# Performance work log

Measured on AMD Instinct MI355X. Metric: run time of the kernel, lower is better.

## Reference

```python
import jax, jax.numpy as jnp
import numpy as np

B, S, DIM = 2, 8192, 1024
NH, NKV, HD = 16, 4, 64
GROUPS = NH // NKV
CHUNK = 128
THETA = 10000.0


def _slopes(h):
    # ALiBi-style per-head decay slopes (h is a power of two)
    return jnp.asarray([2.0 ** (-8.0 / h * (i + 1)) for i in range(h)], dtype=jnp.float32)


def _rope_tables(s, d):
    inv = 1.0 / (THETA ** (np.arange(0, d, 2, dtype=np.float64) / d))
    freqs = np.outer(np.arange(s, dtype=np.float64), inv)  # [s, d/2]
    emb = np.concatenate([freqs, freqs], axis=-1)  # [s, d]
    return jnp.asarray(np.cos(emb), jnp.float32), jnp.asarray(np.sin(emb), jnp.float32)


def _apply_rope(x, cos, sin):
    # x: [b, h, s, d]; cos/sin: [s, d]
    x1, x2 = jnp.split(x, 2, axis=-1)
    rot = jnp.concatenate([-x2, x1], axis=-1)
    return x * cos + rot * sin


def _lightning_attn(q, k, v, slopes, chunk):
    # out[t] = sum_{i<=t} exp(-slope*(t-i)) * (q_t . k_i) * v_i, chunked O(n) recurrence
    b, h, s, d = q.shape
    nc = s // chunk
    t = jnp.arange(chunk, dtype=jnp.float32)
    sl = slopes[:, None, None]  # [h,1,1]
    mask = jnp.where(t[:, None] >= t[None, :],
                     jnp.exp(-sl * (t[:, None] - t[None, :])), 0.0)  # [h,C,C]
    q_dec = jnp.exp(-slopes[:, None] * (t + 1.0))[..., None]          # [h,C,1]
    k_dec = jnp.exp(-slopes[:, None] * (chunk - 1.0 - t))[..., None]  # [h,C,1]
    blk_dec = jnp.exp(-slopes * chunk)[None, :, None, None]           # [1,h,1,1]

    def to_chunks(x):
        return x.reshape(b, h, nc, chunk, d).transpose(2, 0, 1, 3, 4)  # [nc,b,h,C,d]

    qc, kc, vc = to_chunks(q), to_chunks(k), to_chunks(v)

    def step(kv, inp):
        qi, ki, vi = inp  # [b,h,C,d]
        scores = jnp.einsum('bhtd,bhsd->bhts', qi, ki) * mask
        o = jnp.einsum('bhts,bhsd->bhtd', scores, vi) \
            + jnp.einsum('bhtd,bhde->bhte', qi * q_dec, kv)
        kv = blk_dec * kv + jnp.einsum('bhtd,bhte->bhde', ki * k_dec, vi)
        return kv, o

    kv0 = jnp.zeros((b, h, d, d), q.dtype)
    _, outs = jax.lax.scan(step, kv0, (qc, kc, vc))  # outs: [nc,b,h,C,d]
    return outs.transpose(1, 2, 0, 3, 4).reshape(b, h, s, d)


def setup_inputs() -> dict:
    key = jax.random.key(0)
    k0, k1, k2, k3, k4 = jax.random.split(key, 5)
    x = jax.random.normal(k0, (B, S, DIM), jnp.float32)
    Wq = jax.random.normal(k1, (NH * HD, DIM), jnp.float32) * 0.02
    Wk = jax.random.normal(k2, (NKV * HD, DIM), jnp.float32) * 0.02
    Wv = jax.random.normal(k3, (NKV * HD, DIM), jnp.float32) * 0.02
    Wo = jax.random.normal(k4, (DIM, NH * HD), jnp.float32) * 0.02
    return {"x": x, "Wq": Wq, "Wk": Wk, "Wv": Wv, "Wo": Wo}


def reference(x, Wq, Wk, Wv, Wo):
    b, s, _ = x.shape
    q = (x @ Wq.T).reshape(b, s, NH, HD).transpose(0, 2, 1, 3)
    k = (x @ Wk.T).reshape(b, s, NKV, HD).transpose(0, 2, 1, 3)
    v = (x @ Wv.T).reshape(b, s, NKV, HD).transpose(0, 2, 1, 3)
    cos, sin = _rope_tables(s, HD)
    q = _apply_rope(q, cos, sin)
    k = _apply_rope(k, cos, sin)
    # GQA expand: head index = kv_head*groups + g  <=>  repeat along head axis
    k = jnp.repeat(k, GROUPS, axis=1)
    v = jnp.repeat(v, GROUPS, axis=1)
    out = _lightning_attn(q, k, v, _slopes(NH), CHUNK)  # [b,NH,s,HD]
    out = out.transpose(0, 2, 1, 3).reshape(b, s, NH * HD)
    return out @ Wo.T
```

## Files before the change

### kernel.cpp

```cpp
#include <hip/hip_runtime.h>
#include <hip/hip_bf16.h>

#define B_ 2
#define S_ 8192
#define DIM_ 1024
#define NH_ 16
#define NKV_ 4
#define HD_ 64
#define NC_ 64

typedef __bf16 bf16x8 __attribute__((ext_vector_type(8)));
typedef float f32x4 __attribute__((ext_vector_type(4)));
using bf16 = __hip_bfloat16;

#define ASYNC16(gp, lp) __builtin_amdgcn_global_load_lds( \
    (__attribute__((address_space(1))) void*)(void*)(gp), \
    (__attribute__((address_space(3))) void*)(void*)(lp), 16, 0, 0)

__global__ __launch_bounds__(256) void prep_kernel(const float* __restrict__ x, const float* __restrict__ Wq,
                                                   const float* __restrict__ Wk, const float* __restrict__ Wv,
                                                   const float* __restrict__ Wo, bf16* __restrict__ xb,
                                                   bf16* __restrict__ wqkv, bf16* __restrict__ wo,
                                                   float* __restrict__ cosd, float* __restrict__ sind) {
    int bid = blockIdx.x;
    if (bid < 16384) {
        size_t i = ((size_t)bid * 256 + threadIdx.x) * 4;
        const float4 f = *(const float4*)(x + i);
        bf16 t[4];
        t[0] = __float2bfloat16(f.x); t[1] = __float2bfloat16(f.y);
        t[2] = __float2bfloat16(f.z); t[3] = __float2bfloat16(f.w);
        *(uint2*)(xb + i) = *(const uint2*)t;
    } else if (bid < 18944) {
        size_t e = ((size_t)(bid - 16384) * 256 + threadIdx.x) * 4;
        const float* src;
        bf16* dst;
        if (e < 1048576)        { src = Wq + e;             dst = wqkv + e; }
        else if (e < 1310720)   { src = Wk + (e - 1048576); dst = wqkv + e; }
        else if (e < 1572864)   { src = Wv + (e - 1310720); dst = wqkv + e; }
        else                    { src = Wo + (e - 1572864); dst = wo + (e - 1572864); }
        const float4 f = *(const float4*)src;
        bf16 t[4];
        t[0] = __float2bfloat16(f.x); t[1] = __float2bfloat16(f.y);
        t[2] = __float2bfloat16(f.z); t[3] = __float2bfloat16(f.w);
        *(uint2*)dst = *(const uint2*)t;
    } else {
        int idx = (bid - 18944) * 256 + threadIdx.x;
        int s = idx >> 5, i = idx & 31;
        double inv = exp((double)i * (-9.210340371976184 / 32.0));
        double rev = ((double)s * inv) * 0.15915494309189535;
        double frac = rev - floor(rev);
        float a = (float)frac * 6.2831853071795865f;
        cosd[idx] = __cosf(a);
        sind[idx] = __sinf(a);
    }
}

template <typename OT>
__global__ __launch_bounds__(256, 3) void gemm_bt_kernel(const bf16* __restrict__ A, const bf16* __restrict__ Bm,
                                                         OT* __restrict__ C, int M, int N, int K, int rope_ncols,
                                                         const float* __restrict__ cosd,
                                                         const float* __restrict__ sind) {
    __shared__ bf16 As[128 * 64];
    __shared__ bf16 Bs[128 * 64];
    const int tid = threadIdx.x;
    const int bm = blockIdx.x * 128, bn = blockIdx.y * 128;
    const int wave = tid >> 6, lane = tid & 63;
    const int wm = (wave >> 1) * 64, wn = (wave & 1) * 64;
    const int lr = lane & 15, quad = lane >> 4;
    const int srow = wave * 32;
    const int lrow = lane >> 3;
    const int lchunk = ((lane & 7) ^ lrow) * 8;
    const bf16* Ag = A + (size_t)(bm + srow + lrow) * K + lchunk;
    const bf16* Bg = Bm + (size_t)(bn + srow + lrow) * K + lchunk;
    f32x4 acc[4][4] = {};
    for (int k0 = 0; k0 < K; k0 += 64) {
#pragma unroll
        for (int p = 0; p < 4; ++p) {
            ASYNC16(Ag + (size_t)(p * 8) * K + k0, &As[(srow + p * 8) * 64]);
            ASYNC16(Bg + (size_t)(p * 8) * K + k0, &Bs[(srow + p * 8) * 64]);
        }
        __syncthreads();
#pragma unroll
        for (int kk = 0; kk < 64; kk += 32) {
            const int sw = (((kk >> 3) + quad) ^ (lr & 7)) << 3;
            bf16x8 af[4], bfr[4];
#pragma unroll
            for (int i = 0; i < 4; ++i) af[i] = *(const bf16x8*)(&As[(wm + i * 16 + lr) * 64 + sw]);
#pragma unroll
            for (int i = 0; i < 4; ++i) bfr[i] = *(const bf16x8*)(&Bs[(wn + i * 16 + lr) * 64 + sw]);
#pragma unroll
            for (int mi = 0; mi < 4; ++mi)
#pragma unroll
                for (int ni = 0; ni < 4; ++ni)
                    acc[mi][ni] = __builtin_amdgcn_mfma_f32_16x16x32_bf16(af[mi], bfr[ni], acc[mi][ni], 0, 0, 0);
        }
        __syncthreads();
    }
    if (bn + wn < rope_ncols) {
#pragma unroll
        for (int mi = 0; mi < 4; ++mi)
#pragma unroll
            for (int r = 0; r < 4; ++r) {
                int row = bm + wm + mi * 16 + quad * 4 + r;
                int s = row & (S_ - 1);
#pragma unroll
                for (int ni = 0; ni < 2; ++ni) {
                    int i = ni * 16 + lr;
                    float cs = cosd[(s << 5) + i];
                    float sn = sind[(s << 5) + i];
                    float x1 = acc[mi][ni][r], x2 = acc[mi][ni + 2][r];
                    acc[mi][ni][r] = x1 * cs - x2 * sn;
                    acc[mi][ni + 2][r] = x2 * cs + x1 * sn;
                }
            }
    }
#pragma unroll
    for (int mi = 0; mi < 4; ++mi)
#pragma unroll
        for (int ni = 0; ni < 4; ++ni)
#pragma unroll
            for (int r = 0; r < 4; ++r) {
                int row = bm + wm + mi * 16 + quad * 4 + r;
                int col = bn + wn + ni * 16 + lr;
                float v = acc[mi][ni][r];
                if constexpr (__is_same(OT, float)) C[(size_t)row * N + col] = v;
                else C[(size_t)row * N + col] = __float2bfloat16(v);
            }
}


__global__ __launch_bounds__(512) void chunk_kv_kernel(const bf16* __restrict__ qkv, bf16* __restrict__ Cout) {
    const int j = blockIdx.x, g = blockIdx.y, b = blockIdx.z;
    __shared__ bf16 kT[64 * 136];
    __shared__ bf16 vT[64 * 136];
    const int tid = threadIdx.x;
#pragma unroll
    for (int p = 0; p < 2; ++p) {
        int flat = p * 512 + tid;
        int t = flat >> 3, d0 = (flat & 7) * 8;
        const size_t row = (size_t)(b * S_ + j * 128 + t);
        uint4 kw = *(const uint4*)(qkv + row * 1536 + 1024 + g * 64 + d0);
        uint4 vw = *(const uint4*)(qkv + row * 1536 + 1280 + g * 64 + d0);
        const bf16* kp = (const bf16*)&kw;
        const bf16* vp = (const bf16*)&vw;
#pragma unroll
        for (int i = 0; i < 8; ++i) {
            int e = d0 + i;
            int sw = (((t >> 3) & ~7) << 3) + ((((t >> 3) ^ (e >> 3)) & 7) << 3) + (t & 7);
            kT[e * 136 + sw] = kp[i];
            vT[e * 136 + sw] = vp[i];
        }
    }
    __syncthreads();
    const int wave = tid >> 6, lane = tid & 63, lr = lane & 15, quad = lane >> 4;
    const int eblk = (wave & 3) * 16;
    const int hp = (wave >> 2) * 2;
    f32x4 acc[2][4] = {};
    float slope[2], g1[2];
#pragma unroll
    for (int hh = 0; hh < 2; ++hh) {
        slope[hh] = exp2f(-0.5f * (float)(g * 4 + hp + hh + 1));
        g1[hh] = __expf(slope[hh]);
    }
#pragma unroll
    for (int ks = 0; ks < 128; ks += 32) {
        int qa = (ks >> 3) + quad;
        int qhi = (qa & ~7) << 3;
        int ea = eblk + lr;
        bf16x8 a = *(const bf16x8*)(&vT[ea * 136 + qhi + (((qa ^ (ea >> 3)) & 7) << 3)]);
        float av[8];
#pragma unroll
        for (int i = 0; i < 8; ++i) av[i] = (float)a[i];
        bf16x8 bb[4];
#pragma unroll
        for (int ni = 0; ni < 4; ++ni) {
            int eb = ni * 16 + lr;
            bb[ni] = *(const bf16x8*)(&kT[eb * 136 + qhi + (((qa ^ (eb >> 3)) & 7) << 3)]);
        }
#pragma unroll
        for (int hh = 0; hh < 2; ++hh) {
            float m = __expf(-slope[hh] * (float)(127 - ks - quad * 8));
            bf16x8 as;
#pragma unroll
            for (int i = 0; i < 8; ++i) { as[i] = (__bf16)(av[i] * m); m *= g1[hh]; }
#pragma unroll
            for (int ni = 0; ni < 4; ++ni)
                acc[hh][ni] = __builtin_amdgcn_mfma_f32_16x16x32_bf16(as, bb[ni], acc[hh][ni], 0, 0, 0);
        }
    }
#pragma unroll
    for (int hh = 0; hh < 2; ++hh) {
        int h = g * 4 + hp + hh;
        bf16* out = Cout + ((size_t)((b * NH_ + h) * NC_ + j)) * 4096;
#pragma unroll
        for (int ni = 0; ni < 4; ++ni)
#pragma unroll
            for (int r = 0; r < 4; ++r)
                out[(eblk + quad * 4 + r) * 64 + ni * 16 + lr] = __float2bfloat16(acc[hh][ni][r]);
    }
}

__global__ __launch_bounds__(256) void scan_kv_kernel(const bf16* __restrict__ Cin, bf16* __restrict__ st) {
    const int bh = blockIdx.x >> 4;
    const int f = ((blockIdx.x & 15) << 8) + threadIdx.x;
    const int h = bh & (NH_ - 1);
    const float slope = exp2f(-0.5f * (float)(h + 1));
    const float bdec = __expf(-slope * 128.0f);
    const bf16* Cb = Cin + (size_t)bh * NC_ * 4096 + f;
    bf16* sb = st + (size_t)bh * NC_ * 4096 + f;
    float carry = 0.f;
#pragma unroll 8
    for (int c = 0; c < NC_; ++c) {
        sb[(size_t)c * 4096] = __float2bfloat16(carry);
        carry = bdec * carry + __bfloat162float(Cb[(size_t)c * 4096]);
    }
}

__global__ __launch_bounds__(256, 3) void attn_chunk_kernel(const bf16* __restrict__ qkv,
                                                            const bf16* __restrict__ kvst,
                                                            bf16* __restrict__ outb) {
    const int c = blockIdx.x, h = blockIdx.y, b = blockIdx.z;
    const int g = h >> 2;
    const float slope = exp2f(-0.5f * (float)(h + 1));
    __shared__ bf16 smem[26112];
    bf16* qs  = smem;
    bf16* kbs = smem + 8192;
    bf16* Ps  = smem;
    bf16* vT  = smem + 17408;
    const int tid = threadIdx.x;
    const int wave = tid >> 6, lane = tid & 63, lr = lane & 15, quad = lane >> 4;
    const int srow = lane >> 3;
    const int schunk = ((lane & 7) ^ srow) * 8;
#pragma unroll
    for (int p = 0; p < 4; ++p) {
        int t0 = wave * 8 + p * 32;
        size_t row = (size_t)(b * S_ + c * 128 + t0 + srow);
        ASYNC16(qkv + row * 1536 + h * 64 + schunk, &qs[t0 * 64]);
        ASYNC16(qkv + row * 1536 + 1024 + g * 64 + schunk, &kbs[t0 * 64]);
    }
    asm volatile("s_waitcnt vmcnt(0)");
    __syncthreads();
    const int m0 = wave * 32;
    f32x4 sacc[2][8] = {};
#pragma unroll
    for (int kk = 0; kk < 64; kk += 32) {
        const int sw = ((((kk >> 3) + quad) ^ (lr & 7)) & 7) << 3;
        bf16x8 af0 = *(const bf16x8*)(&qs[(m0 + lr) * 64 + sw]);
        bf16x8 af1 = *(const bf16x8*)(&qs[(m0 + 16 + lr) * 64 + sw]);
#pragma unroll
        for (int ni = 0; ni < 8; ++ni) {
            bf16x8 bfr = *(const bf16x8*)(&kbs[(ni * 16 + lr) * 64 + sw]);
            sacc[0][ni] = __builtin_amdgcn_mfma_f32_16x16x32_bf16(af0, bfr, sacc[0][ni], 0, 0, 0);
            sacc[1][ni] = __builtin_amdgcn_mfma_f32_16x16x32_bf16(af1, bfr, sacc[1][ni], 0, 0, 0);
        }
    }
    f32x4 oacc[2][4] = {};
    const bf16* kvb = kvst + ((size_t)((b * NH_ + h) * NC_ + c)) * 4096;
    float qd0 = __expf(-slope * (float)(m0 + lr + 1));
    float qd1 = __expf(-slope * (float)(m0 + 16 + lr + 1));
#pragma unroll
    for (int kk = 0; kk < 64; kk += 32) {
        const int sw = ((((kk >> 3) + quad) ^ (lr & 7)) & 7) << 3;
        bf16x8 a0 = *(const bf16x8*)(&qs[(m0 + lr) * 64 + sw]);
        bf16x8 a1 = *(const bf16x8*)(&qs[(m0 + 16 + lr) * 64 + sw]);
#pragma unroll
        for (int i = 0; i < 8; ++i) {
            a0[i] = (__bf16)((float)a0[i] * qd0);
            a1[i] = (__bf16)((float)a1[i] * qd1);
        }
#pragma unroll
        for (int ni = 0; ni < 4; ++ni) {
            bf16x8 bk = *(const bf16x8*)(kvb + (ni * 16 + lr) * 64 + kk + quad * 8);
            oacc[0][ni] = __builtin_amdgcn_mfma_f32_16x16x32_bf16(a0, bk, oacc[0][ni], 0, 0, 0);
            oacc[1][ni] = __builtin_amdgcn_mfma_f32_16x16x32_bf16(a1, bk, oacc[1][ni], 0, 0, 0);
        }
    }
    __syncthreads();
    float ftv[2][4], gtv[8];
#pragma unroll
    for (int mi = 0; mi < 2; ++mi)
#pragma unroll
        for (int r = 0; r < 4; ++r) ftv[mi][r] = __expf(-slope * (float)(mi * 16 + quad * 4 + r));
#pragma unroll
    for (int ni = 0; ni < 8; ++ni)
        gtv[ni] = __expf(-slope * fmaxf((float)(m0 - (ni * 16 + lr)), -31.0f));
#pragma unroll
    for (int mi = 0; mi < 2; ++mi)
#pragma unroll
        for (int ni = 0; ni < 8; ++ni)
#pragma unroll
            for (int r = 0; r < 4; ++r) {
                int t = m0 + mi * 16 + quad * 4 + r;
                int tp = ni * 16 + lr;
                float val = (t >= tp) ? sacc[mi][ni][r] * ftv[mi][r] * gtv[ni] : 0.f;
                int sw = (((tp >> 3) & ~7) << 3) + ((((tp >> 3) ^ (t >> 3)) & 7) << 3) + (tp & 7);
                Ps[t * 136 + sw] = __float2bfloat16(val);
            }
#pragma unroll
    for (int p = 0; p < 4; ++p) {
        int flat = p * 256 + tid;
        int t = flat >> 3, d0 = (flat & 7) * 8;
        size_t row = (size_t)(b * S_ + c * 128 + t);
        uint4 vw = *(const uint4*)(qkv + row * 1536 + 1280 + g * 64 + d0);
        const bf16* vp = (const bf16*)&vw;
#pragma unroll
        for (int i = 0; i < 8; ++i) {
            int e = d0 + i;
            int sw = (((t >> 3) & ~7) << 3) + ((((t >> 3) ^ (e >> 3)) & 7) << 3) + (t & 7);
            vT[e * 136 + sw] = vp[i];
        }
    }
    __syncthreads();
#pragma unroll
    for (int ks2 = 0; ks2 < 128; ks2 += 32) {
        int qa = (ks2 >> 3) + quad;
        int qhi = (qa & ~7) << 3;
        int ra0 = m0 + lr, ra1 = m0 + 16 + lr;
        bf16x8 af0 = *(const bf16x8*)(&Ps[ra0 * 136 + qhi + (((qa ^ (ra0 >> 3)) & 7) << 3)]);
        bf16x8 af1 = *(const bf16x8*)(&Ps[ra1 * 136 + qhi + (((qa ^ (ra1 >> 3)) & 7) << 3)]);
#pragma unroll
        for (int ni = 0; ni < 4; ++ni) {
            int eb = ni * 16 + lr;
            bf16x8 bfv = *(const bf16x8*)(&vT[eb * 136 + qhi + (((qa ^ (eb >> 3)) & 7) << 3)]);
            oacc[0][ni] = __builtin_amdgcn_mfma_f32_16x16x32_bf16(af0, bfv, oacc[0][ni], 0, 0, 0);
            oacc[1][ni] = __builtin_amdgcn_mfma_f32_16x16x32_bf16(af1, bfv, oacc[1][ni], 0, 0, 0);
        }
    }
#pragma unroll
    for (int mi = 0; mi < 2; ++mi)
#pragma unroll
        for (int ni = 0; ni < 4; ++ni)
#pragma unroll
            for (int r = 0; r < 4; ++r) {
                int t = m0 + mi * 16 + quad * 4 + r;
                int e = ni * 16 + lr;
                size_t row = (size_t)(b * S_ + c * 128 + t);
                outb[row * (NH_ * 64) + h * 64 + e] = __float2bfloat16(oacc[mi][ni][r]);
            }
}

extern "C" void kernel_launch(void* const* d_in, const int* in_sizes, int n_in,
                              void* d_out, int out_size, void* d_ws, size_t ws_size,
                              hipStream_t stream) {
    (void)in_sizes; (void)n_in; (void)out_size; (void)ws_size;
    const float* x  = (const float*)d_in[0];
    const float* Wq = (const float*)d_in[1];
    const float* Wk = (const float*)d_in[2];
    const float* Wv = (const float*)d_in[3];
    const float* Wo = (const float*)d_in[4];
    float* out = (float*)d_out;
    char* ws = (char*)d_ws;
    bf16*  xb    = (bf16*)(ws);
    bf16*  qkvb  = (bf16*)(ws + 33554432);
    bf16*  wqkvb = (bf16*)(ws + 83886080);
    bf16*  wob   = (bf16*)(ws + 87031808);
    float* cosd  = (float*)(ws + 89128960);
    float* sind  = (float*)(ws + 90177536);
    bf16*  Cbuf  = (bf16*)(ws + 91226112);
    bf16*  kvst  = (bf16*)(ws + 108003328);
    bf16*  attn  = xb;

    prep_kernel<<<19968, 256, 0, stream>>>(x, Wq, Wk, Wv, Wo, xb, wqkvb, wob, cosd, sind);

    gemm_bt_kernel<bf16><<<dim3(128, 12), 256, 0, stream>>>(xb, wqkvb, qkvb, 16384, 1536, 1024, 1280, cosd, sind);

    chunk_kv_kernel<<<dim3(NC_, NKV_, B_), 512, 0, stream>>>(qkvb, Cbuf);
    scan_kv_kernel<<<512, 256, 0, stream>>>(Cbuf, kvst);
    attn_chunk_kernel<<<dim3(NC_, NH_, B_), 256, 0, stream>>>(qkvb, kvst, attn);

    gemm_bt_kernel<float><<<dim3(128, 8), 256, 0, stream>>>(attn, wob, out, 16384, 1024, 1024, 0, cosd, sind);
}
```

Before: 264.1 us.

## Split attn chunk kernel across 8 waves with 16-row tiles and early V prefetch

```diff
diff --git a/kernel.cpp b/kernel.cpp
--- a/kernel.cpp
+++ b/kernel.cpp
@@ -216,7 +216,7 @@
     }
 }
 
-__global__ __launch_bounds__(256, 3) void attn_chunk_kernel(const bf16* __restrict__ qkv,
+__global__ __launch_bounds__(512, 2) void attn_chunk_kernel(const bf16* __restrict__ qkv,
                                                             const bf16* __restrict__ kvst,
                                                             bf16* __restrict__ outb) {
     const int c = blockIdx.x, h = blockIdx.y, b = blockIdx.z;
@@ -231,78 +231,74 @@
     const int wave = tid >> 6, lane = tid & 63, lr = lane & 15, quad = lane >> 4;
     const int srow = lane >> 3;
     const int schunk = ((lane & 7) ^ srow) * 8;
-#pragma unroll
-    for (int p = 0; p < 4; ++p) {
-        int t0 = wave * 8 + p * 32;
+    uint4 vreg[2];
+#pragma unroll
+    for (int p = 0; p < 2; ++p) {
+        int flat = p * 512 + tid;
+        int t = flat >> 3, d0 = (flat & 7) * 8;
+        size_t row = (size_t)(b * S_ + c * 128 + t);
+        vreg[p] = *(const uint4*)(qkv + row * 1536 + 1280 + g * 64 + d0);
+    }
+#pragma unroll
+    for (int p = 0; p < 2; ++p) {
+        int t0 = (wave + p * 8) * 8;
         size_t row = (size_t)(b * S_ + c * 128 + t0 + srow);
         ASYNC16(qkv + row * 1536 + h * 64 + schunk, &qs[t0 * 64]);
         ASYNC16(qkv + row * 1536 + 1024 + g * 64 + schunk, &kbs[t0 * 64]);
     }
     asm volatile("s_waitcnt vmcnt(0)");
     __syncthreads();
-    const int m0 = wave * 32;
-    f32x4 sacc[2][8] = {};
-#pragma unroll
-    for (int kk = 0; kk < 64; kk += 32) {
-        const int sw = ((((kk >> 3) + quad) ^ (lr & 7)) & 7) << 3;
-        bf16x8 af0 = *(const bf16x8*)(&qs[(m0 + lr) * 64 + sw]);
-        bf16x8 af1 = *(const bf16x8*)(&qs[(m0 + 16 + lr) * 64 + sw]);
+    const int m0 = wave * 16;
+    bf16x8 qf[2];
+#pragma unroll
+    for (int kk = 0; kk < 2; ++kk)
+        qf[kk] = *(const bf16x8*)(&qs[(m0 + lr) * 64 + ((((kk * 4 + quad)) ^ (lr & 7)) & 7) * 8]);
+    f32x4 sacc[8] = {};
+#pragma unroll
+    for (int kk = 0; kk < 2; ++kk) {
+        const int sw = (((kk * 4 + quad) ^ (lr & 7)) & 7) << 3;
 #pragma unroll
         for (int ni = 0; ni < 8; ++ni) {
             bf16x8 bfr = *(const bf16x8*)(&kbs[(ni * 16 + lr) * 64 + sw]);
-            sacc[0][ni] = __builtin_amdgcn_mfma_f32_16x16x32_bf16(af0, bfr, sacc[0][ni], 0, 0, 0);
-            sacc[1][ni] = __builtin_amdgcn_mfma_f32_16x16x32_bf16(af1, bfr, sacc[1][ni], 0, 0, 0);
-        }
-    }
-    f32x4 oacc[2][4] = {};
+            sacc[ni] = __builtin_amdgcn_mfma_f32_16x16x32_bf16(qf[kk], bfr, sacc[ni], 0, 0, 0);
+        }
+    }
+    f32x4 oacc[4] = {};
     const bf16* kvb = kvst + ((size_t)((b * NH_ + h) * NC_ + c)) * 4096;
-    float qd0 = __expf(-slope * (float)(m0 + lr + 1));
-    float qd1 = __expf(-slope * (float)(m0 + 16 + lr + 1));
-#pragma unroll
-    for (int kk = 0; kk < 64; kk += 32) {
-        const int sw = ((((kk >> 3) + quad) ^ (lr & 7)) & 7) << 3;
-        bf16x8 a0 = *(const bf16x8*)(&qs[(m0 + lr) * 64 + sw]);
-        bf16x8 a1 = *(const bf16x8*)(&qs[(m0 + 16 + lr) * 64 + sw]);
-#pragma unroll
-        for (int i = 0; i < 8; ++i) {
-            a0[i] = (__bf16)((float)a0[i] * qd0);
-            a1[i] = (__bf16)((float)a1[i] * qd1);
-        }
+    float qd = __expf(-slope * (float)(m0 + lr + 1));
+#pragma unroll
+    for (int kk = 0; kk < 2; ++kk) {
+        bf16x8 a0;
+#pragma unroll
+        for (int i = 0; i < 8; ++i) a0[i] = (__bf16)((float)qf[kk][i] * qd);
 #pragma unroll
         for (int ni = 0; ni < 4; ++ni) {
-            bf16x8 bk = *(const bf16x8*)(kvb + (ni * 16 + lr) * 64 + kk + quad * 8);
-            oacc[0][ni] = __builtin_amdgcn_mfma_f32_16x16x32_bf16(a0, bk, oacc[0][ni], 0, 0, 0);
-            oacc[1][ni] = __builtin_amdgcn_mfma_f32_16x16x32_bf16(a1, bk, oacc[1][ni], 0, 0, 0);
+            bf16x8 bk = *(const bf16x8*)(kvb + (ni * 16 + lr) * 64 + kk * 32 + quad * 8);
+            oacc[ni] = __builtin_amdgcn_mfma_f32_16x16x32_bf16(a0, bk, oacc[ni], 0, 0, 0);
         }
     }
     __syncthreads();
-    float ftv[2][4], gtv[8];
-#pragma unroll
-    for (int mi = 0; mi < 2; ++mi)
-#pragma unroll
-        for (int r = 0; r < 4; ++r) ftv[mi][r] = __expf(-slope * (float)(mi * 16 + quad * 4 + r));
+    float ftv[4], gtv[8];
+#pragma unroll
+    for (int r = 0; r < 4; ++r) ftv[r] = __expf(-slope * (float)(quad * 4 + r));
 #pragma unroll
     for (int ni = 0; ni < 8; ++ni)
-        gtv[ni] = __expf(-slope * fmaxf((float)(m0 - (ni * 16 + lr)), -31.0f));
-#pragma unroll
-    for (int mi = 0; mi < 2; ++mi)
-#pragma unroll
-        for (int ni = 0; ni < 8; ++ni)
-#pragma unroll
-            for (int r = 0; r < 4; ++r) {
-                int t = m0 + mi * 16 + quad * 4 + r;
-                int tp = ni * 16 + lr;
-                float val = (t >= tp) ? sacc[mi][ni][r] * ftv[mi][r] * gtv[ni] : 0.f;
-                int sw = (((tp >> 3) & ~7) << 3) + ((((tp >> 3) ^ (t >> 3)) & 7) << 3) + (tp & 7);
-                Ps[t * 136 + sw] = __float2bfloat16(val);
-            }
-#pragma unroll
-    for (int p = 0; p < 4; ++p) {
-        int flat = p * 256 + tid;
+        gtv[ni] = __expf(-slope * fmaxf((float)(m0 - (ni * 16 + lr)), -15.0f));
+#pragma unroll
+    for (int ni = 0; ni < 8; ++ni)
+#pragma unroll
+        for (int r = 0; r < 4; ++r) {
+            int t = m0 + quad * 4 + r;
+            int tp = ni * 16 + lr;
+            float val = (t >= tp) ? sacc[ni][r] * ftv[r] * gtv[ni] : 0.f;
+            int sw = (((tp >> 3) & ~7) << 3) + ((((tp >> 3) ^ (t >> 3)) & 7) << 3) + (tp & 7);
+            Ps[t * 136 + sw] = __float2bfloat16(val);
+        }
+#pragma unroll
+    for (int p = 0; p < 2; ++p) {
+        int flat = p * 512 + tid;
         int t = flat >> 3, d0 = (flat & 7) * 8;
-        size_t row = (size_t)(b * S_ + c * 128 + t);
-        uint4 vw = *(const uint4*)(qkv + row * 1536 + 1280 + g * 64 + d0);
-        const bf16* vp = (const bf16*)&vw;
+        const bf16* vp = (const bf16*)&vreg[p];
 #pragma unroll
         for (int i = 0; i < 8; ++i) {
             int e = d0 + i;
@@ -315,28 +311,24 @@
     for (int ks2 = 0; ks2 < 128; ks2 += 32) {
         int qa = (ks2 >> 3) + quad;
         int qhi = (qa & ~7) << 3;
-        int ra0 = m0 + lr, ra1 = m0 + 16 + lr;
+        int ra0 = m0 + lr;
         bf16x8 af0 = *(const bf16x8*)(&Ps[ra0 * 136 + qhi + (((qa ^ (ra0 >> 3)) & 7) << 3)]);
-        bf16x8 af1 = *(const bf16x8*)(&Ps[ra1 * 136 + qhi + (((qa ^ (ra1 >> 3)) & 7) << 3)]);
 #pragma unroll
         for (int ni = 0; ni < 4; ++ni) {
             int eb = ni * 16 + lr;
             bf16x8 bfv = *(const bf16x8*)(&vT[eb * 136 + qhi + (((qa ^ (eb >> 3)) & 7) << 3)]);
-            oacc[0][ni] = __builtin_amdgcn_mfma_f32_16x16x32_bf16(af0, bfv, oacc[0][ni], 0, 0, 0);
-            oacc[1][ni] = __builtin_amdgcn_mfma_f32_16x16x32_bf16(af1, bfv, oacc[1][ni], 0, 0, 0);
-        }
-    }
-#pragma unroll
-    for (int mi = 0; mi < 2; ++mi)
-#pragma unroll
-        for (int ni = 0; ni < 4; ++ni)
-#pragma unroll
-            for (int r = 0; r < 4; ++r) {
-                int t = m0 + mi * 16 + quad * 4 + r;
-                int e = ni * 16 + lr;
-                size_t row = (size_t)(b * S_ + c * 128 + t);
-                outb[row * (NH_ * 64) + h * 64 + e] = __float2bfloat16(oacc[mi][ni][r]);
-            }
+            oacc[ni] = __builtin_amdgcn_mfma_f32_16x16x32_bf16(af0, bfv, oacc[ni], 0, 0, 0);
+        }
+    }
+#pragma unroll
+    for (int ni = 0; ni < 4; ++ni)
+#pragma unroll
+        for (int r = 0; r < 4; ++r) {
+            int t = m0 + quad * 4 + r;
+            int e = ni * 16 + lr;
+            size_t row = (size_t)(b * S_ + c * 128 + t);
+            outb[row * (NH_ * 64) + h * 64 + e] = __float2bfloat16(oacc[ni][r]);
+        }
 }
 
 extern "C" void kernel_launch(void* const* d_in, const int* in_sizes, int n_in,
@@ -366,7 +358,7 @@
 
     chunk_kv_kernel<<<dim3(NC_, NKV_, B_), 512, 0, stream>>>(qkvb, Cbuf);
     scan_kv_kernel<<<512, 256, 0, stream>>>(Cbuf, kvst);
-    attn_chunk_kernel<<<dim3(NC_, NH_, B_), 256, 0, stream>>>(qkvb, kvst, attn);
+    attn_chunk_kernel<<<dim3(NC_, NH_, B_), 512, 0, stream>>>(qkvb, kvst, attn);
 
     gemm_bt_kernel<float><<<dim3(128, 8), 256, 0, stream>>>(attn, wob, out, 16384, 1024, 1024, 0, cosd, sind);
 }
```

After: 280.0 us. 1.06x slower.
